# Kernel tuning notes

Hardware: AMD Instinct MI355X
Metric: run time of the kernel (lower is better)

## Reference

```python
import jax, jax.numpy as jnp
import numpy as np

N = 100000   # nodes
E = 1600000  # edges (avg degree 16)
IN, HID, OUT = 128, 128, 64
EPS = 1e-5


def setup_inputs() -> dict:
    key = jax.random.key(0)
    ks = jax.random.split(key, 16)
    x = jax.random.normal(ks[0], (N, IN), jnp.float32)
    edge_index = jax.random.randint(ks[1], (2, E), 0, N, dtype=jnp.int64)
    edge_weight = jax.random.uniform(ks[2], (E,), jnp.float32)

    def lin(k, o, i):
        return jax.random.normal(k, (o, i), jnp.float32) / np.float32(np.sqrt(i))

    return {
        "x": x, "edge_index": edge_index, "edge_weight": edge_weight,
        # SGConv linear layers
        "W1": lin(ks[3], HID, IN), "b1": jnp.zeros((HID,), jnp.float32),
        "W2": lin(ks[4], HID, HID), "b2": jnp.zeros((HID,), jnp.float32),
        "W3": lin(ks[5], OUT, HID), "b3": jnp.zeros((OUT,), jnp.float32),
        # BatchNorm affine params (nontrivial values for a meaningful reference)
        "g1": 1.0 + 0.1 * jax.random.normal(ks[6], (HID,), jnp.float32),
        "be1": 0.1 * jax.random.normal(ks[7], (HID,), jnp.float32),
        "g2": 1.0 + 0.1 * jax.random.normal(ks[8], (HID,), jnp.float32),
        "be2": 0.1 * jax.random.normal(ks[9], (HID,), jnp.float32),
        # proj MLP
        "pW1": lin(ks[10], HID, HID), "pb1": jnp.zeros((HID,), jnp.float32),
        "pW2": lin(ks[11], HID, HID), "pb2": jnp.zeros((HID,), jnp.float32),
    }


def reference(x, edge_index, edge_weight, W1, b1, W2, b2, W3, b3,
              g1, be1, g2, be2, pW1, pb1, pW2, pb2):
    src, dst = edge_index[0], edge_index[1]

    def propagate(h):
        # SGConv K=1, normalize=False: edge-weighted scatter-sum over neighbors
        msg = h[src] * edge_weight[:, None]          # [E, d]
        return jax.ops.segment_sum(msg, dst, num_segments=N)

    def bn(h, g, b):
        # BatchNorm1d, training-mode batch statistics (biased variance)
        m = h.mean(axis=0)
        v = h.var(axis=0)
        return (h - m) * jax.lax.rsqrt(v + EPS) * g + b

    h = x
    h = propagate(h) @ W1.T + b1
    h = jax.nn.relu(bn(h, g1, be1))                  # dropout = identity (eval)
    h = propagate(h) @ W2.T + b2
    h = jax.nn.relu(bn(h, g2, be2))

    # proj: Linear -> Dropout(identity) -> ReLU -> Linear
    z = jax.nn.relu(h @ pW1.T + pb1) @ pW2.T + pb2
    logits = propagate(h) @ W3.T + b3
    return (logits, h, z)
```

## Files before the change

kernel.cpp:

```cpp
#include <hip/hip_runtime.h>


#define NF 128

using short8   = __attribute__((ext_vector_type(8))) short;
using ushort8v = __attribute__((ext_vector_type(8))) unsigned short;
using f32x4    = __attribute__((ext_vector_type(4))) float;

__device__ __forceinline__ float b2f(unsigned short u) {
    return __uint_as_float(((unsigned)u) << 16);
}
__device__ __forceinline__ unsigned short f2b(float f) {
    unsigned u = __float_as_uint(f);
    u += 0x7fff + ((u >> 16) & 1);
    return (unsigned short)(u >> 16);
}

__global__ __launch_bounds__(256) void bhist_k(const int* __restrict__ ei,
                                               int* __restrict__ bhist,
                                               int E, int nbuk)
{
    __shared__ int cnt[512];
    int t = threadIdx.x;
    cnt[t] = 0; cnt[t + 256] = 0;
    __syncthreads();
    int e0 = blockIdx.x * 2048;
    int eend = min(e0 + 2048, E);
    for (int i = e0 + t; i < eend; i += 256)
        atomicAdd(&cnt[ei[E + i] >> 8], 1);
    __syncthreads();
    for (int b = t; b < nbuk; b += 256) {
        int c = cnt[b];
        if (c) atomicAdd(&bhist[b], c);
    }
}

__global__ __launch_bounds__(512) void bscan_k(const int* __restrict__ bhist,
                                               int* __restrict__ bbase,
                                               int* __restrict__ bcur, int nbuk)
{
    __shared__ int sc[512];
    int t = threadIdx.x;
    int v = (t < nbuk) ? bhist[t] : 0;
    sc[t] = v;
    __syncthreads();
    for (int ofs = 1; ofs < 512; ofs <<= 1) {
        int x = (t >= ofs) ? sc[t - ofs] : 0;
        __syncthreads();
        sc[t] += x;
        __syncthreads();
    }
    if (t < nbuk) {
        int ex = sc[t] - v;
        bbase[t] = ex;
        bcur[t]  = ex;
    }
}

__global__ __launch_bounds__(256) void filla_k(const int* __restrict__ ei,
                                               const float* __restrict__ ew,
                                               int* __restrict__ bcur,
                                               int2* __restrict__ tmp, int E)
{
    __shared__ int dstg[2048];
    __shared__ int cnt[512];
    __shared__ int base[512];
    int t = threadIdx.x;
    cnt[t] = 0; cnt[t + 256] = 0;
    __syncthreads();
    int e0 = blockIdx.x * 2048;
    int eend = min(e0 + 2048, E);
    int n = eend - e0;
    for (int i = t; i < n; i += 256) {
        int d = ei[E + e0 + i];
        dstg[i] = d;
        atomicAdd(&cnt[d >> 8], 1);
    }
    __syncthreads();
    for (int b = t; b < 512; b += 256) {
        int c = cnt[b];
        base[b] = c ? atomicAdd(&bcur[b], c) : 0;
        cnt[b] = 0;
    }
    __syncthreads();
    for (int i = t; i < n; i += 256) {
        int d = dstg[i];
        int b = d >> 8;
        int r = atomicAdd(&cnt[b], 1);
        int2 q;
        q.x = (int)(((unsigned)ei[e0 + i]) | (((unsigned)(d & 255)) << 24));
        q.y = __float_as_int(ew[e0 + i]);
        tmp[base[b] + r] = q;
    }
}

__global__ __launch_bounds__(512) void fillb_k(const int2* __restrict__ tmp,
                                               const int* __restrict__ bbase,
                                               int* __restrict__ off,
                                               int2* __restrict__ epk,
                                               int N, int E, int nbuk)
{
    __shared__ int lcnt[256];
    __shared__ int lcur[256];
    int t = threadIdx.x;
    int b = blockIdx.x;
    int lo = b << 8;
    int nn = min(256, N - lo);
    if (t < 256) lcnt[t] = 0;
    __syncthreads();
    int s = bbase[b];
    int e_end = (b + 1 < nbuk) ? bbase[b + 1] : E;
    for (int i = s + t; i < e_end; i += 512)
        atomicAdd(&lcnt[((unsigned)tmp[i].x) >> 24], 1);
    __syncthreads();
    int v = (t < 256) ? lcnt[t] : 0;
    for (int ofs = 1; ofs < 256; ofs <<= 1) {
        int x = (t >= ofs && t < 256) ? lcnt[t - ofs] : 0;
        __syncthreads();
        if (t < 256) lcnt[t] += x;
        __syncthreads();
    }
    if (t < 256) {
        int st = s + lcnt[t] - v;
        lcur[t] = st;
        if (t < nn) off[lo + t] = st;
    }
    if (b == 0 && t == 0) off[N] = E;
    __syncthreads();
    for (int i = s + t; i < e_end; i += 512) {
        int2 q = tmp[i];
        unsigned qx = (unsigned)q.x;
        int pos = atomicAdd(&lcur[qx >> 24], 1);
        int2 o;
        o.x = (int)(qx & 0xFFFFFF);
        o.y = q.y;
        epk[pos] = o;
    }
}

__global__ __launch_bounds__(256) void convx_k(const float* __restrict__ x,
                                               unsigned short* __restrict__ xb,
                                               int total4)
{
    int idx = blockIdx.x * 256 + threadIdx.x;
    if (idx >= total4) return;
    float4 v = *(const float4*)&x[(size_t)idx * 4];
    ushort4 o;
    o.x = f2b(v.x); o.y = f2b(v.y); o.z = f2b(v.z); o.w = f2b(v.w);
    *(ushort4*)&xb[(size_t)idx * 4] = o;
}

__global__ __launch_bounds__(64) void convw_k(const float* __restrict__ W,
                                              unsigned short* __restrict__ Wb)
{
    int lane = threadIdx.x;
    int nb = blockIdx.x >> 2, ks = blockIdx.x & 3;
    const float* src = W + (size_t)(nb * 16 + (lane & 15)) * 128 + ks * 32 + (lane >> 4) * 8;
    unsigned short* dst = Wb + ((size_t)blockIdx.x * 64 + lane) * 8;
#pragma unroll
    for (int j = 0; j < 8; j++) dst[j] = f2b(src[j]);
}

template <int BN>
__global__ __launch_bounds__(256) void gather_k(
    const unsigned short* __restrict__ h, const int* __restrict__ off,
    const int2* __restrict__ epk, unsigned short* __restrict__ p, int N,
    const float* __restrict__ bnstats, const float* __restrict__ g,
    const float* __restrict__ be, float invN)
{
    int row = blockIdx.x * 4 + (threadIdx.x >> 6);
    if (row >= N) return;
    int lane = threadIdx.x & 63;
    int half = lane >> 4;
    int sub  = lane & 15;
    int c0 = sub * 8;

    float sc[8], sh[8];
#pragma unroll
    for (int j = 0; j < 8; j++) { sc[j] = 1.f; sh[j] = 0.f; }
    if (BN) {
#pragma unroll
        for (int j = 0; j < 8; j++) {
            float m = bnstats[c0 + j] * invN;
            float v = bnstats[NF + c0 + j] * invN - m * m;
            float r = rsqrtf(v + 1e-5f) * g[c0 + j];
            sc[j] = r; sh[j] = be[c0 + j] - m * r;
        }
    }

    int beg = off[row], end = off[row + 1];
    float a[8];
#pragma unroll
    for (int j = 0; j < 8; j++) a[j] = 0.f;

#define PROC_EDGE(qq, uu)                                                     \
    {                                                                         \
        float w = __int_as_float((qq).y);                                     \
        _Pragma("unroll")                                                     \
        for (int j = 0; j < 8; j++) {                                         \
            float v = b2f((unsigned short)(uu)[j]);                           \
            if (BN) v = fmaxf(fmaf(v, sc[j], sh[j]), 0.f);                    \
            a[j] = fmaf(v, w, a[j]);                                          \
        }                                                                     \
    }

    int e = beg;
    for (; e + 16 <= end; e += 16) {
        int2 q0 = epk[e + 0 + half],  q1 = epk[e + 4 + half];
        int2 q2 = epk[e + 8 + half],  q3 = epk[e + 12 + half];
        ushort8v u0 = *(const ushort8v*)&h[(size_t)q0.x * NF + c0];
        ushort8v u1 = *(const ushort8v*)&h[(size_t)q1.x * NF + c0];
        ushort8v u2 = *(const ushort8v*)&h[(size_t)q2.x * NF + c0];
        ushort8v u3 = *(const ushort8v*)&h[(size_t)q3.x * NF + c0];
        PROC_EDGE(q0, u0); PROC_EDGE(q1, u1);
        PROC_EDGE(q2, u2); PROC_EDGE(q3, u3);
    }
    for (; e + 4 <= end; e += 4) {
        int2 q = epk[e + half];
        ushort8v u = *(const ushort8v*)&h[(size_t)q.x * NF + c0];
        PROC_EDGE(q, u);
    }
    if (half < end - e) {
        int2 q = epk[e + half];
        ushort8v u = *(const ushort8v*)&h[(size_t)q.x * NF + c0];
        PROC_EDGE(q, u);
    }
#undef PROC_EDGE

#pragma unroll
    for (int j = 0; j < 8; j++) {
        a[j] += __shfl_xor(a[j], 16);
        a[j] += __shfl_xor(a[j], 32);
    }

    if (half == 0) {
        ushort8v o;
#pragma unroll
        for (int j = 0; j < 8; j++) o[j] = f2b(a[j]);
        *(ushort8v*)&p[(size_t)row * NF + c0] = o;
    }
}

__global__ __launch_bounds__(256) void gather64_k(
    const unsigned short* __restrict__ y, const int* __restrict__ off,
    const int2* __restrict__ epk, const float* __restrict__ bias,
    float* __restrict__ out, int N)
{
    int row = blockIdx.x * 8 + (threadIdx.x >> 5);
    if (row >= N) return;
    int l32 = threadIdx.x & 31;
    int str = l32 >> 4;
    int sub = l32 & 15;
    int c0 = sub * 4;

    int beg = off[row], end = off[row + 1];
    float a[4] = {0.f, 0.f, 0.f, 0.f};

#define PROC_E64(qq, uu)                                                      \
    {                                                                         \
        float w = __int_as_float((qq).y);                                     \
        a[0] = fmaf(b2f((uu).x), w, a[0]);                                    \
        a[1] = fmaf(b2f((uu).y), w, a[1]);                                    \
        a[2] = fmaf(b2f((uu).z), w, a[2]);                                    \
        a[3] = fmaf(b2f((uu).w), w, a[3]);                                    \
    }

    int e = beg;
    for (; e + 8 <= end; e += 8) {
        int2 q0 = epk[e + 0 + str], q1 = epk[e + 2 + str];
        int2 q2 = epk[e + 4 + str], q3 = epk[e + 6 + str];
        ushort4 u0 = *(const ushort4*)&y[(size_t)q0.x * 64 + c0];
        ushort4 u1 = *(const ushort4*)&y[(size_t)q1.x * 64 + c0];
        ushort4 u2 = *(const ushort4*)&y[(size_t)q2.x * 64 + c0];
        ushort4 u3 = *(const ushort4*)&y[(size_t)q3.x * 64 + c0];
        PROC_E64(q0, u0); PROC_E64(q1, u1);
        PROC_E64(q2, u2); PROC_E64(q3, u3);
    }
    for (; e + 2 <= end; e += 2) {
        int2 q = epk[e + str];
        ushort4 u = *(const ushort4*)&y[(size_t)q.x * 64 + c0];
        PROC_E64(q, u);
    }
    if (str == 0 && e < end) {
        int2 q = epk[e];
        ushort4 u = *(const ushort4*)&y[(size_t)q.x * 64 + c0];
        PROC_E64(q, u);
    }
#undef PROC_E64

#pragma unroll
    for (int j = 0; j < 4; j++) a[j] += __shfl_xor(a[j], 16);

    if (str == 0) {
        float4 o;
        o.x = a[0] + bias[c0];     o.y = a[1] + bias[c0 + 1];
        o.z = a[2] + bias[c0 + 2]; o.w = a[3] + bias[c0 + 3];
        *(float4*)&out[(size_t)row * 64 + c0] = o;
    }
}

template <int M, int COUT>
__global__ __launch_bounds__(256) void mgemm_k(
    const unsigned short* __restrict__ A, const unsigned short* __restrict__ Wb,
    const float* __restrict__ bias, void* __restrict__ Cp,
    int N, int relu, float* __restrict__ stats)
{
    constexpr int MI = (M == 128) ? 4 : 2;
    __shared__ float sbuf[256];

    const int tid = threadIdx.x, wid = tid >> 6, lane = tid & 63;
    const int quad = lane >> 4, l16 = lane & 15;
    const int rowBase = blockIdx.x * 128;
    int r0, c0;
    if constexpr (M == 128) { r0 = (wid >> 1) * 64; c0 = (wid & 1) * 64; }
    else                    { r0 = wid * 32;        c0 = 0; }

    f32x4 acc[MI][4];
#pragma unroll
    for (int mi = 0; mi < MI; mi++)
#pragma unroll
        for (int ni = 0; ni < 4; ni++)
#pragma unroll
            for (int r = 0; r < 4; r++) acc[mi][ni][r] = 0.f;

#pragma unroll
    for (int ks = 0; ks < 4; ++ks) {
        short8 af[MI], bf[4];
#pragma unroll
        for (int mi = 0; mi < MI; mi++) {
            int gr = rowBase + r0 + mi * 16 + l16;
            gr = (gr < N) ? gr : (N - 1);
            af[mi] = *(const short8*)(A + (size_t)gr * 128 + ks * 32 + quad * 8);
        }
#pragma unroll
        for (int ni = 0; ni < 4; ni++) {
            int nb = (c0 >> 4) + ni;
            bf[ni] = *(const short8*)(Wb + ((size_t)(nb * 4 + ks) * 64 + lane) * 8);
        }
#pragma unroll
        for (int mi = 0; mi < MI; mi++)
#pragma unroll
            for (int ni = 0; ni < 4; ni++)
                acc[mi][ni] = __builtin_amdgcn_mfma_f32_16x16x32_bf16(
                    af[mi], bf[ni], acc[mi][ni], 0, 0, 0);
    }

    float csum[4] = {0.f, 0.f, 0.f, 0.f}, csq[4] = {0.f, 0.f, 0.f, 0.f};
#pragma unroll
    for (int mi = 0; mi < MI; mi++) {
#pragma unroll
        for (int r = 0; r < 4; r++) {
            int gr = rowBase + r0 + mi * 16 + quad * 4 + r;
            if (gr >= N) continue;
#pragma unroll
            for (int ni = 0; ni < 4; ni++) {
                int col = c0 + ni * 16 + l16;
                float v = acc[mi][ni][r] + (bias ? bias[col] : 0.f);
                if (relu) v = fmaxf(v, 0.f);
                if constexpr (COUT == 1)
                    ((unsigned short*)Cp)[(size_t)gr * M + col] = f2b(v);
                else
                    ((float*)Cp)[(size_t)gr * M + col] = v;
                csum[ni] += v;
                csq[ni]  += v * v;
            }
        }
    }

    if (stats) {
        sbuf[tid] = 0.f;
        __syncthreads();
#pragma unroll
        for (int ni = 0; ni < 4; ni++) {
            int col = c0 + ni * 16 + l16;
            atomicAdd(&sbuf[col], csum[ni]);
            atomicAdd(&sbuf[128 + col], csq[ni]);
        }
        __syncthreads();
        if (tid < 128) {
            unsafeAtomicAdd(&stats[tid], sbuf[tid]);
            unsafeAtomicAdd(&stats[NF + tid], sbuf[128 + tid]);
        }
    }
}

__global__ __launch_bounds__(256) void bnrelu2_k(
    const unsigned short* __restrict__ pre, const float* __restrict__ stats,
    const float* __restrict__ g, const float* __restrict__ be,
    float* __restrict__ outh, unsigned short* __restrict__ hb,
    int total4, float invN)
{
    int idx = blockIdx.x * 256 + threadIdx.x;
    if (idx >= total4) return;
    int c = (idx * 4) & 127;
    ushort4 u = *(const ushort4*)&pre[(size_t)idx * 4];
    float in[4] = {b2f(u.x), b2f(u.y), b2f(u.z), b2f(u.w)};
    float o[4];
#pragma unroll
    for (int i = 0; i < 4; i++) {
        float m   = stats[c + i] * invN;
        float var = stats[NF + c + i] * invN - m * m;
        float rs  = rsqrtf(var + 1e-5f);
        o[i] = fmaxf((in[i] - m) * rs * g[c + i] + be[c + i], 0.f);
    }
    float4 f; f.x = o[0]; f.y = o[1]; f.z = o[2]; f.w = o[3];
    *(float4*)&outh[(size_t)idx * 4] = f;
    ushort4 h4;
    h4.x = f2b(o[0]); h4.y = f2b(o[1]); h4.z = f2b(o[2]); h4.w = f2b(o[3]);
    *(ushort4*)&hb[(size_t)idx * 4] = h4;
}

__global__ __launch_bounds__(256) void projf_k(
    const unsigned short* __restrict__ A, const unsigned short* __restrict__ W1b,
    const float* __restrict__ bias1, const unsigned short* __restrict__ W2b,
    const float* __restrict__ bias2, float* __restrict__ Z, int N)
{
    __shared__ unsigned short tbuf[128][136];

    const int tid = threadIdx.x, wid = tid >> 6, lane = tid & 63;
    const int quad = lane >> 4, l16 = lane & 15;
    const int rowBase = blockIdx.x * 128;
    const int r0 = (wid >> 1) * 64, c0 = (wid & 1) * 64;

    f32x4 acc[4][4];
#pragma unroll
    for (int mi = 0; mi < 4; mi++)
#pragma unroll
        for (int ni = 0; ni < 4; ni++)
#pragma unroll
            for (int r = 0; r < 4; r++) acc[mi][ni][r] = 0.f;

#pragma unroll
    for (int ks = 0; ks < 4; ++ks) {
        short8 af[4], bf[4];
#pragma unroll
        for (int mi = 0; mi < 4; mi++) {
            int gr = rowBase + r0 + mi * 16 + l16;
            gr = (gr < N) ? gr : (N - 1);
            af[mi] = *(const short8*)(A + (size_t)gr * 128 + ks * 32 + quad * 8);
        }
#pragma unroll
        for (int ni = 0; ni < 4; ni++) {
            int nb = (c0 >> 4) + ni;
            bf[ni] = *(const short8*)(W1b + ((size_t)(nb * 4 + ks) * 64 + lane) * 8);
        }
#pragma unroll
        for (int mi = 0; mi < 4; mi++)
#pragma unroll
            for (int ni = 0; ni < 4; ni++)
                acc[mi][ni] = __builtin_amdgcn_mfma_f32_16x16x32_bf16(
                    af[mi], bf[ni], acc[mi][ni], 0, 0, 0);
    }
#pragma unroll
    for (int mi = 0; mi < 4; mi++)
#pragma unroll
        for (int r = 0; r < 4; r++) {
            int lr = r0 + mi * 16 + quad * 4 + r;
#pragma unroll
            for (int ni = 0; ni < 4; ni++) {
                int col = c0 + ni * 16 + l16;
                float v = fmaxf(acc[mi][ni][r] + bias1[col], 0.f);
                tbuf[lr][col] = f2b(v);
            }
        }
    __syncthreads();

#pragma unroll
    for (int mi = 0; mi < 4; mi++)
#pragma unroll
        for (int ni = 0; ni < 4; ni++)
#pragma unroll
            for (int r = 0; r < 4; r++) acc[mi][ni][r] = 0.f;

#pragma unroll
    for (int ks = 0; ks < 4; ++ks) {
        short8 af[4], bf[4];
#pragma unroll
        for (int mi = 0; mi < 4; mi++)
            af[mi] = *(const short8*)&tbuf[r0 + mi * 16 + l16][ks * 32 + quad * 8];
#pragma unroll
        for (int ni = 0; ni < 4; ni++) {
            int nb = (c0 >> 4) + ni;
            bf[ni] = *(const short8*)(W2b + ((size_t)(nb * 4 + ks) * 64 + lane) * 8);
        }
#pragma unroll
        for (int mi = 0; mi < 4; mi++)
#pragma unroll
            for (int ni = 0; ni < 4; ni++)
                acc[mi][ni] = __builtin_amdgcn_mfma_f32_16x16x32_bf16(
                    af[mi], bf[ni], acc[mi][ni], 0, 0, 0);
    }
#pragma unroll
    for (int mi = 0; mi < 4; mi++)
#pragma unroll
        for (int r = 0; r < 4; r++) {
            int gr = rowBase + r0 + mi * 16 + quad * 4 + r;
            if (gr >= N) continue;
#pragma unroll
            for (int ni = 0; ni < 4; ni++) {
                int col = c0 + ni * 16 + l16;
                Z[(size_t)gr * 128 + col] = acc[mi][ni][r] + bias2[col];
            }
        }
}

extern "C" void kernel_launch(void* const* d_in, const int* in_sizes, int n_in,
                              void* d_out, int out_size, void* d_ws, size_t ws_size,
                              hipStream_t stream)
{
    const float* x   = (const float*)d_in[0];
    const int*   ei  = (const int*)d_in[1];
    const float* ew  = (const float*)d_in[2];
    const float* W1  = (const float*)d_in[3];
    const float* b1  = (const float*)d_in[4];
    const float* W2  = (const float*)d_in[5];
    const float* b2  = (const float*)d_in[6];
    const float* W3  = (const float*)d_in[7];
    const float* b3  = (const float*)d_in[8];
    const float* g1  = (const float*)d_in[9];
    const float* be1 = (const float*)d_in[10];
    const float* g2  = (const float*)d_in[11];
    const float* be2 = (const float*)d_in[12];
    const float* pW1 = (const float*)d_in[13];
    const float* pb1 = (const float*)d_in[14];
    const float* pW2 = (const float*)d_in[15];
    const float* pb2 = (const float*)d_in[16];

    const int N = in_sizes[0] / NF;
    const int E = in_sizes[2];

    float* out_logits = (float*)d_out;
    float* out_h      = out_logits + (size_t)N * 64;
    float* out_z      = out_h + (size_t)N * NF;

    const size_t rowsUS = (size_t)N * NF;
    int2*           epk = (int2*)d_ws;
    unsigned short* B1  = (unsigned short*)(epk + E);
    unsigned short* B2  = B1 + rowsUS;
    unsigned short* B3  = B2 + rowsUS;
    float* stats1 = (float*)(B3 + rowsUS);
    float* stats2 = stats1 + 256;
    float* wconv  = stats2 + 256;
    unsigned short* W1b  = (unsigned short*)wconv;
    unsigned short* W2b  = W1b + 128 * 128;
    unsigned short* pW1b = W2b + 128 * 128;
    unsigned short* pW2b = pW1b + 128 * 128;
    unsigned short* W3b  = pW2b + 128 * 128;
    int* off   = (int*)(W3b + 64 * 128);
    int* bhist = off + N + 1;
    int* bbase = bhist + 512;
    int* bcur  = bbase + 512;
    int2* tmp  = (int2*)B2;

    const int nbuk   = (N + 255) >> 8;
    const int ggrid  = (N + 127) / 128;
    const int pgrid  = (N + 3) / 4;
    const int p8grid = (N + 7) / 8;
    const int c4grid = (N * NF / 4 + 255) / 256;
    const int egrid  = (E + 2047) / 2048;
    const float invN = 1.f / (float)N;

    convx_k<<<c4grid, 256, 0, stream>>>(x, B1, N * NF / 4);
    convw_k<<<32, 64, 0, stream>>>(W1, W1b);
    convw_k<<<32, 64, 0, stream>>>(W2, W2b);
    convw_k<<<32, 64, 0, stream>>>(pW1, pW1b);
    convw_k<<<32, 64, 0, stream>>>(pW2, pW2b);
    convw_k<<<16, 64, 0, stream>>>(W3, W3b);

    hipMemsetAsync(bhist, 0, 512 * sizeof(int), stream);
    bhist_k<<<egrid, 256, 0, stream>>>(ei, bhist, E, nbuk);
    bscan_k<<<1, 512, 0, stream>>>(bhist, bbase, bcur, nbuk);
    filla_k<<<egrid, 256, 0, stream>>>(ei, ew, bcur, tmp, E);
    fillb_k<<<nbuk, 512, 0, stream>>>(tmp, bbase, off, epk, N, E, nbuk);

    gather_k<0><<<pgrid, 256, 0, stream>>>(B1, off, epk, B2, N,
                                           nullptr, nullptr, nullptr, 0.f);
    hipMemsetAsync(stats1, 0, 2 * NF * sizeof(float), stream);
    mgemm_k<128, 1><<<ggrid, 256, 0, stream>>>(B2, W1b, b1, B3, N, 0, stats1);

    gather_k<1><<<pgrid, 256, 0, stream>>>(B3, off, epk, B2, N,
                                           stats1, g1, be1, invN);
    hipMemsetAsync(stats2, 0, 2 * NF * sizeof(float), stream);
    mgemm_k<128, 1><<<ggrid, 256, 0, stream>>>(B2, W2b, b2, B1, N, 0, stats2);

    bnrelu2_k<<<c4grid, 256, 0, stream>>>(B1, stats2, g2, be2, out_h, B2,
                                          N * NF / 4, invN);

    mgemm_k<64, 1><<<ggrid, 256, 0, stream>>>(B2, W3b, nullptr, B3, N, 0, nullptr);
    gather64_k<<<p8grid, 256, 0, stream>>>(B3, off, epk, b3, out_logits, N);

    projf_k<<<ggrid, 256, 0, stream>>>(B2, pW1b, pb1, pW2b, pb2, out_z, N);
}
```

Baseline: 647.2 us.

## Drop histogram pass via fixed-capacity buckets, merge weight conversions and memsets

Measured after the change: 589.3 us. 9.0% less time.

```diff
diff --git a/kernel.cpp b/kernel.cpp
--- a/kernel.cpp
+++ b/kernel.cpp
@@ -2,6 +2,7 @@
 
 
 #define NF 128
+#define BCAP 6144
 
 using short8   = __attribute__((ext_vector_type(8))) short;
 using ushort8v = __attribute__((ext_vector_type(8))) unsigned short;
@@ -16,74 +17,34 @@
     return (unsigned short)(u >> 16);
 }
 
-__global__ __launch_bounds__(256) void bhist_k(const int* __restrict__ ei,
-                                               int* __restrict__ bhist,
-                                               int E, int nbuk)
-{
-    __shared__ int cnt[512];
-    int t = threadIdx.x;
-    cnt[t] = 0; cnt[t + 256] = 0;
-    __syncthreads();
-    int e0 = blockIdx.x * 2048;
-    int eend = min(e0 + 2048, E);
-    for (int i = e0 + t; i < eend; i += 256)
-        atomicAdd(&cnt[ei[E + i] >> 8], 1);
-    __syncthreads();
-    for (int b = t; b < nbuk; b += 256) {
-        int c = cnt[b];
-        if (c) atomicAdd(&bhist[b], c);
-    }
-}
-
-__global__ __launch_bounds__(512) void bscan_k(const int* __restrict__ bhist,
-                                               int* __restrict__ bbase,
-                                               int* __restrict__ bcur, int nbuk)
-{
-    __shared__ int sc[512];
-    int t = threadIdx.x;
-    int v = (t < nbuk) ? bhist[t] : 0;
-    sc[t] = v;
-    __syncthreads();
-    for (int ofs = 1; ofs < 512; ofs <<= 1) {
-        int x = (t >= ofs) ? sc[t - ofs] : 0;
-        __syncthreads();
-        sc[t] += x;
-        __syncthreads();
-    }
-    if (t < nbuk) {
-        int ex = sc[t] - v;
-        bbase[t] = ex;
-        bcur[t]  = ex;
-    }
-}
-
-__global__ __launch_bounds__(256) void filla_k(const int* __restrict__ ei,
-                                               const float* __restrict__ ew,
-                                               int* __restrict__ bcur,
-                                               int2* __restrict__ tmp, int E)
-{
-    __shared__ int dstg[2048];
+
+__global__ __launch_bounds__(512) void filla2_k(const int* __restrict__ ei,
+                                                const float* __restrict__ ew,
+                                                int* __restrict__ bcur,
+                                                int2* __restrict__ tmp, int E)
+{
+    __shared__ int dstg[4096];
     __shared__ int cnt[512];
     __shared__ int base[512];
     int t = threadIdx.x;
-    cnt[t] = 0; cnt[t + 256] = 0;
-    __syncthreads();
-    int e0 = blockIdx.x * 2048;
-    int eend = min(e0 + 2048, E);
+    cnt[t] = 0;
+    __syncthreads();
+    int e0 = blockIdx.x * 4096;
+    int eend = min(e0 + 4096, E);
     int n = eend - e0;
-    for (int i = t; i < n; i += 256) {
+    for (int i = t; i < n; i += 512) {
         int d = ei[E + e0 + i];
         dstg[i] = d;
         atomicAdd(&cnt[d >> 8], 1);
     }
     __syncthreads();
-    for (int b = t; b < 512; b += 256) {
-        int c = cnt[b];
-        base[b] = c ? atomicAdd(&bcur[b], c) : 0;
-        cnt[b] = 0;
-    }
-    __syncthreads();
-    for (int i = t; i < n; i += 256) {
+    {
+        int c = cnt[t];
+        base[t] = c ? (t * BCAP + atomicAdd(&bcur[t], c)) : 0;
+        cnt[t] = 0;
+    }
+    __syncthreads();
+    for (int i = t; i < n; i += 512) {
         int d = dstg[i];
         int b = d >> 8;
         int r = atomicAdd(&cnt[b], 1);
@@ -94,8 +55,26 @@
     }
 }
 
+__global__ __launch_bounds__(512) void bscan_k(const int* __restrict__ bcnt,
+                                               int* __restrict__ bbase, int nbuk)
+{
+    __shared__ int sc[512];
+    int t = threadIdx.x;
+    int v = (t < nbuk) ? bcnt[t] : 0;
+    sc[t] = v;
+    __syncthreads();
+    for (int ofs = 1; ofs < 512; ofs <<= 1) {
+        int x = (t >= ofs) ? sc[t - ofs] : 0;
+        __syncthreads();
+        sc[t] += x;
+        __syncthreads();
+    }
+    if (t < nbuk) bbase[t] = sc[t] - v;
+}
+
 __global__ __launch_bounds__(512) void fillb_k(const int2* __restrict__ tmp,
                                                const int* __restrict__ bbase,
+                                               const int* __restrict__ bcnt,
                                                int* __restrict__ off,
                                                int2* __restrict__ epk,
                                                int N, int E, int nbuk)
@@ -108,10 +87,11 @@
     int nn = min(256, N - lo);
     if (t < 256) lcnt[t] = 0;
     __syncthreads();
+    const int2* src = tmp + (size_t)b * BCAP;
+    int cntb = bcnt[b];
     int s = bbase[b];
-    int e_end = (b + 1 < nbuk) ? bbase[b + 1] : E;
-    for (int i = s + t; i < e_end; i += 512)
-        atomicAdd(&lcnt[((unsigned)tmp[i].x) >> 24], 1);
+    for (int i = t; i < cntb; i += 512)
+        atomicAdd(&lcnt[((unsigned)src[i].x) >> 24], 1);
     __syncthreads();
     int v = (t < 256) ? lcnt[t] : 0;
     for (int ofs = 1; ofs < 256; ofs <<= 1) {
@@ -127,8 +107,8 @@
     }
     if (b == 0 && t == 0) off[N] = E;
     __syncthreads();
-    for (int i = s + t; i < e_end; i += 512) {
-        int2 q = tmp[i];
+    for (int i = t; i < cntb; i += 512) {
+        int2 q = src[i];
         unsigned qx = (unsigned)q.x;
         int pos = atomicAdd(&lcur[qx >> 24], 1);
         int2 o;
@@ -150,13 +130,25 @@
     *(ushort4*)&xb[(size_t)idx * 4] = o;
 }
 
-__global__ __launch_bounds__(64) void convw_k(const float* __restrict__ W,
-                                              unsigned short* __restrict__ Wb)
-{
+__global__ __launch_bounds__(64) void convw_all_k(
+    const float* __restrict__ W1,  const float* __restrict__ W2,
+    const float* __restrict__ pW1, const float* __restrict__ pW2,
+    const float* __restrict__ W3,
+    unsigned short* __restrict__ W1b,  unsigned short* __restrict__ W2b,
+    unsigned short* __restrict__ pW1b, unsigned short* __restrict__ pW2b,
+    unsigned short* __restrict__ W3b)
+{
+    int bid = blockIdx.x;
+    const float* W; unsigned short* Wb; int lb;
+    if      (bid < 32)  { W = W1;  Wb = W1b;  lb = bid; }
+    else if (bid < 64)  { W = W2;  Wb = W2b;  lb = bid - 32; }
+    else if (bid < 96)  { W = pW1; Wb = pW1b; lb = bid - 64; }
+    else if (bid < 128) { W = pW2; Wb = pW2b; lb = bid - 96; }
+    else                { W = W3;  Wb = W3b;  lb = bid - 128; }
     int lane = threadIdx.x;
-    int nb = blockIdx.x >> 2, ks = blockIdx.x & 3;
+    int nb = lb >> 2, ks = lb & 3;
     const float* src = W + (size_t)(nb * 16 + (lane & 15)) * 128 + ks * 32 + (lane >> 4) * 8;
-    unsigned short* dst = Wb + ((size_t)blockIdx.x * 64 + lane) * 8;
+    unsigned short* dst = Wb + ((size_t)lb * 64 + lane) * 8;
 #pragma unroll
     for (int j = 0; j < 8; j++) dst[j] = f2b(src[j]);
 }
@@ -246,11 +238,11 @@
     const int2* __restrict__ epk, const float* __restrict__ bias,
     float* __restrict__ out, int N)
 {
-    int row = blockIdx.x * 8 + (threadIdx.x >> 5);
+    int row = blockIdx.x * 4 + (threadIdx.x >> 6);
     if (row >= N) return;
-    int l32 = threadIdx.x & 31;
-    int str = l32 >> 4;
-    int sub = l32 & 15;
+    int lane = threadIdx.x & 63;
+    int str = lane >> 4;
+    int sub = lane & 15;
     int c0 = sub * 4;
 
     int beg = off[row], end = off[row + 1];
@@ -266,9 +258,9 @@
     }
 
     int e = beg;
-    for (; e + 8 <= end; e += 8) {
-        int2 q0 = epk[e + 0 + str], q1 = epk[e + 2 + str];
-        int2 q2 = epk[e + 4 + str], q3 = epk[e + 6 + str];
+    for (; e + 16 <= end; e += 16) {
+        int2 q0 = epk[e + 0 + str],  q1 = epk[e + 4 + str];
+        int2 q2 = epk[e + 8 + str],  q3 = epk[e + 12 + str];
         ushort4 u0 = *(const ushort4*)&y[(size_t)q0.x * 64 + c0];
         ushort4 u1 = *(const ushort4*)&y[(size_t)q1.x * 64 + c0];
         ushort4 u2 = *(const ushort4*)&y[(size_t)q2.x * 64 + c0];
@@ -276,22 +268,25 @@
         PROC_E64(q0, u0); PROC_E64(q1, u1);
         PROC_E64(q2, u2); PROC_E64(q3, u3);
     }
-    for (; e + 2 <= end; e += 2) {
+    for (; e + 4 <= end; e += 4) {
         int2 q = epk[e + str];
         ushort4 u = *(const ushort4*)&y[(size_t)q.x * 64 + c0];
         PROC_E64(q, u);
     }
-    if (str == 0 && e < end) {
-        int2 q = epk[e];
+    if (str < end - e) {
+        int2 q = epk[e + str];
         ushort4 u = *(const ushort4*)&y[(size_t)q.x * 64 + c0];
         PROC_E64(q, u);
     }
 #undef PROC_E64
 
 #pragma unroll
-    for (int j = 0; j < 4; j++) a[j] += __shfl_xor(a[j], 16);
-
-    if (str == 0) {
+    for (int j = 0; j < 4; j++) {
+        a[j] += __shfl_xor(a[j], 16);
+        a[j] += __shfl_xor(a[j], 32);
+    }
+
+    if (lane < 16) {
         float4 o;
         o.x = a[0] + bias[c0];     o.y = a[1] + bias[c0 + 1];
         o.z = a[2] + bias[c0 + 2]; o.w = a[3] + bias[c0 + 3];
@@ -540,54 +535,46 @@
     unsigned short* B3  = B2 + rowsUS;
     float* stats1 = (float*)(B3 + rowsUS);
     float* stats2 = stats1 + 256;
-    float* wconv  = stats2 + 256;
-    unsigned short* W1b  = (unsigned short*)wconv;
+    int*   bcur   = (int*)(stats2 + 256);
+    int*   bbase  = bcur + 512;
+    unsigned short* W1b  = (unsigned short*)(bbase + 512);
     unsigned short* W2b  = W1b + 128 * 128;
     unsigned short* pW1b = W2b + 128 * 128;
     unsigned short* pW2b = pW1b + 128 * 128;
     unsigned short* W3b  = pW2b + 128 * 128;
-    int* off   = (int*)(W3b + 64 * 128);
-    int* bhist = off + N + 1;
-    int* bbase = bhist + 512;
-    int* bcur  = bbase + 512;
-    int2* tmp  = (int2*)B2;
+    int* off = (int*)(W3b + 64 * 128);
+    int2* tmp = (int2*)B2;
 
     const int nbuk   = (N + 255) >> 8;
     const int ggrid  = (N + 127) / 128;
     const int pgrid  = (N + 3) / 4;
-    const int p8grid = (N + 7) / 8;
     const int c4grid = (N * NF / 4 + 255) / 256;
-    const int egrid  = (E + 2047) / 2048;
+    const int e4grid = (E + 4095) / 4096;
     const float invN = 1.f / (float)N;
 
+    hipMemsetAsync(stats1, 0, (2 * 256) * sizeof(float) + 512 * sizeof(int), stream);
+
     convx_k<<<c4grid, 256, 0, stream>>>(x, B1, N * NF / 4);
-    convw_k<<<32, 64, 0, stream>>>(W1, W1b);
-    convw_k<<<32, 64, 0, stream>>>(W2, W2b);
-    convw_k<<<32, 64, 0, stream>>>(pW1, pW1b);
-    convw_k<<<32, 64, 0, stream>>>(pW2, pW2b);
-    convw_k<<<16, 64, 0, stream>>>(W3, W3b);
-
-    hipMemsetAsync(bhist, 0, 512 * sizeof(int), stream);
-    bhist_k<<<egrid, 256, 0, stream>>>(ei, bhist, E, nbuk);
-    bscan_k<<<1, 512, 0, stream>>>(bhist, bbase, bcur, nbuk);
-    filla_k<<<egrid, 256, 0, stream>>>(ei, ew, bcur, tmp, E);
-    fillb_k<<<nbuk, 512, 0, stream>>>(tmp, bbase, off, epk, N, E, nbuk);
+    convw_all_k<<<176, 64, 0, stream>>>(W1, W2, pW1, pW2, W3,
+                                        W1b, W2b, pW1b, pW2b, W3b);
+
+    filla2_k<<<e4grid, 512, 0, stream>>>(ei, ew, bcur, tmp, E);
+    bscan_k<<<1, 512, 0, stream>>>(bcur, bbase, nbuk);
+    fillb_k<<<nbuk, 512, 0, stream>>>(tmp, bbase, bcur, off, epk, N, E, nbuk);
 
     gather_k<0><<<pgrid, 256, 0, stream>>>(B1, off, epk, B2, N,
                                            nullptr, nullptr, nullptr, 0.f);
-    hipMemsetAsync(stats1, 0, 2 * NF * sizeof(float), stream);
     mgemm_k<128, 1><<<ggrid, 256, 0, stream>>>(B2, W1b, b1, B3, N, 0, stats1);
 
     gather_k<1><<<pgrid, 256, 0, stream>>>(B3, off, epk, B2, N,
                                            stats1, g1, be1, invN);
-    hipMemsetAsync(stats2, 0, 2 * NF * sizeof(float), stream);
     mgemm_k<128, 1><<<ggrid, 256, 0, stream>>>(B2, W2b, b2, B1, N, 0, stats2);
 
     bnrelu2_k<<<c4grid, 256, 0, stream>>>(B1, stats2, g2, be2, out_h, B2,
                                           N * NF / 4, invN);
 
     mgemm_k<64, 1><<<ggrid, 256, 0, stream>>>(B2, W3b, nullptr, B3, N, 0, nullptr);
-    gather64_k<<<p8grid, 256, 0, stream>>>(B3, off, epk, b3, out_logits, N);
+    gather64_k<<<pgrid, 256, 0, stream>>>(B3, off, epk, b3, out_logits, N);
 
     projf_k<<<ggrid, 256, 0, stream>>>(B2, pW1b, pb1, pW2b, pb2, out_z, N);
 }
```
